# Optimization experiments

Measured on AMD Instinct MI355X. Metric: run time of the kernel, lower is better.

## Reference

```python
import jax, jax.numpy as jnp
import numpy as np

INPUT_DIM, DK, DV = 1024, 128, 128


def setup_inputs() -> dict:
    key = jax.random.key(0)
    ks = jax.random.split(key, 7)
    s = 0.02
    return {
        "x": jax.random.normal(ks[0], (4, 4096, INPUT_DIM), dtype=jnp.float32),
        "Wq": jax.random.normal(ks[1], (INPUT_DIM, DK), dtype=jnp.float32) * s,
        "bq": jnp.zeros((DK,), dtype=jnp.float32),
        "Wk": jax.random.normal(ks[2], (INPUT_DIM, DK), dtype=jnp.float32) * s,
        "bk": jnp.zeros((DK,), dtype=jnp.float32),
        "Wv": jax.random.normal(ks[3], (INPUT_DIM, DV), dtype=jnp.float32) * s,
        "bv": jnp.zeros((DV,), dtype=jnp.float32),
    }


def reference(x, Wq, bq, Wk, bk, Wv, bv):
    # single-head self-attention with explicit QK^T softmax V
    scale = DK ** (-0.5)
    q = x @ Wq + bq          # [b, s, dk]
    k = x @ Wk + bk          # [b, s, dk]
    v = x @ Wv + bv          # [b, s, dv]
    scores = jnp.einsum("bqd,bkd->bqk", q, k) * scale  # [b, s, s]
    attn = jax.nn.softmax(scores, axis=-1)
    return jnp.einsum("bqk,bkd->bqd", attn, v)  # [b, s, dv]
```

## Files before the change

### kernel.cpp

```cpp
#include <hip/hip_runtime.h>
#include <hip/hip_bf16.h>
#include <math.h>
#include <stdint.h>


#define SM_SCALE2 0.1275310225216245f

using f32x4  = __attribute__((ext_vector_type(4))) float;
using f32x16 = __attribute__((ext_vector_type(16))) float;
using bf16x8 = __attribute__((ext_vector_type(8))) short;
using s16x4  = __attribute__((ext_vector_type(4))) short;

#define GLD16(gp, lp) __builtin_amdgcn_global_load_lds(                      \
    (const __attribute__((address_space(1))) void*)(gp),                     \
    (__attribute__((address_space(3))) void*)(lp), 16, 0, 0)

__device__ __forceinline__ short f2bf(float f) {
  union { __hip_bfloat16 h; short s; } u;
  u.h = __float2bfloat16(f);
  return u.s;
}

__global__ __launch_bounds__(256) void wprep_k(const float* __restrict__ Wq,
                                               const float* __restrict__ Wk,
                                               const float* __restrict__ Wv,
                                               short* __restrict__ Wt) {
  int tid = blockIdx.x * 256 + threadIdx.x;
  int mat = tid >> 17;
  int r   = tid & 131071;
  int k   = r >> 7;
  int col = r & 127;
  const float* W = (mat == 0) ? Wq : ((mat == 1) ? Wk : Wv);
  Wt[mat * 131072 + col * 1024 + k] = f2bf(W[k * 128 + col]);
}

__global__ __launch_bounds__(256) void proj_k(const float* __restrict__ x,
                                              const short* __restrict__ Wt,
                                              const float* __restrict__ bq,
                                              const float* __restrict__ bk,
                                              const float* __restrict__ bv,
                                              short* __restrict__ Qb,
                                              short* __restrict__ Kb,
                                              short* __restrict__ Vt) {
  const int r0  = blockIdx.x * 32;
  const int tid  = threadIdx.x;
  const int lane = tid & 63;
  const int w    = tid >> 6;
  const int g    = lane >> 4;
  const int l15  = lane & 15;

  __shared__ __align__(16) char smem[57344];
  const char* Wtb = (const char*)Wt;

  f32x4 acc[3][2][2];
  #pragma unroll
  for (int m = 0; m < 3; ++m)
    #pragma unroll
    for (int rb = 0; rb < 2; ++rb)
      #pragma unroll
      for (int cb = 0; cb < 2; ++cb) acc[m][rb][cb] = (f32x4){0.f, 0.f, 0.f, 0.f};

  const int xrow = tid >> 3;
  const int xsl  = tid & 7;

#define XS(B) (smem + (B) * 4096)
#define WTB   (smem + 8192)

#define STAGE_W(T) do {                                                       \
    _Pragma("unroll")                                                         \
    for (int m = 0; m < 3; ++m)                                               \
      _Pragma("unroll")                                                       \
      for (int c = 0; c < 4; ++c) {                                           \
        const int o  = w * 4096 + c * 1024 + lane * 16;                       \
        const int cr = o >> 7;                                                \
        const int cb = (o >> 4) & 7;                                          \
        GLD16(Wtb + m * 262144 + (size_t)cr * 2048 + (T) * 128 +              \
                  ((cb ^ (cr & 7)) << 4),                                     \
              WTB + m * 16384 + w * 4096 + c * 1024);                         \
      }                                                                       \
  } while (0)

#define LOADX(FX, T) do {                                                     \
    _Pragma("unroll")                                                         \
    for (int p = 0; p < 2; ++p) {                                             \
      const int s = xsl + 8 * p;                                              \
      FX[p] = *(const float4*)(x + (size_t)(r0 + xrow) * 1024 + (T) * 64 + s * 4); \
    }                                                                         \
  } while (0)

#define WRITEX(B, FX) do {                                                    \
    char* xb_ = XS(B);                                                        \
    _Pragma("unroll")                                                         \
    for (int p = 0; p < 2; ++p) {                                             \
      const int s = xsl + 8 * p;                                              \
      s16x4 h = { f2bf(FX[p].x), f2bf(FX[p].y), f2bf(FX[p].z), f2bf(FX[p].w) }; \
      *(s16x4*)(xb_ + xrow * 128 + (((s >> 1) ^ (xrow & 7)) << 4) +           \
                ((s & 1) << 3)) = h;                                          \
    }                                                                         \
  } while (0)

  {
    float4 fx0[2];
    LOADX(fx0, 0);
    WRITEX(0, fx0);
  }
  __syncthreads();
  STAGE_W(0);
  __syncthreads();

  for (int t = 0; t < 16; ++t) {
    const int cur = t & 1;
    float4 fx[2];
    if (t < 15) LOADX(fx, t + 1);

    const char* xb = XS(cur);
    #pragma unroll
    for (int kc = 0; kc < 2; ++kc) {
      bf16x8 a[2];
      #pragma unroll
      for (int rb = 0; rb < 2; ++rb)
        a[rb] = *(const bf16x8*)(xb + (rb * 16 + l15) * 128 +
                                 ((((kc << 2) + g) ^ (l15 & 7)) << 4));
      #pragma unroll
      for (int m = 0; m < 3; ++m)
        #pragma unroll
        for (int cb = 0; cb < 2; ++cb) {
          const int col = w * 32 + cb * 16 + l15;
          bf16x8 b = *(const bf16x8*)(WTB + m * 16384 + col * 128 +
                                      ((((kc << 2) + g) ^ (col & 7)) << 4));
          #pragma unroll
          for (int rb = 0; rb < 2; ++rb)
            acc[m][rb][cb] = __builtin_amdgcn_mfma_f32_16x16x32_bf16(a[rb], b,
                                                                     acc[m][rb][cb], 0, 0, 0);
        }
    }

    if (t < 15) {
      WRITEX(cur ^ 1, fx);
      __syncthreads();
      STAGE_W(t + 1);
      __syncthreads();
    }
  }
#undef STAGE_W
#undef LOADX
#undef WRITEX
#undef XS
#undef WTB

  #pragma unroll
  for (int m = 0; m < 2; ++m) {
    short* dst = (m == 0) ? Qb : Kb;
    const float* bias = (m == 0) ? bq : bk;
    #pragma unroll
    for (int cb = 0; cb < 2; ++cb) {
      const int col = w * 32 + cb * 16 + l15;
      const float bc = bias[col];
      #pragma unroll
      for (int rb = 0; rb < 2; ++rb)
        #pragma unroll
        for (int r = 0; r < 4; ++r) {
          float v = acc[m][rb][cb][r] + bc;
          if (m == 0) v *= SM_SCALE2;
          dst[(size_t)(r0 + rb * 16 + (g << 2) + r) * 128 + col] = f2bf(v);
        }
    }
  }
  __syncthreads();
  {
    short* tb = (short*)smem;
    #pragma unroll
    for (int cb = 0; cb < 2; ++cb) {
      const int col = w * 32 + cb * 16 + l15;
      const float bc = bv[col];
      #pragma unroll
      for (int rb = 0; rb < 2; ++rb)
        #pragma unroll
        for (int r = 0; r < 4; ++r)
          tb[col * 40 + rb * 16 + (g << 2) + r] = f2bf(acc[2][rb][cb][r] + bc);
    }
    __syncthreads();
    const int bb = r0 >> 12;
    const int s0 = r0 & 4095;
    const int d  = tid >> 1;
    #pragma unroll
    for (int j = 0; j < 2; ++j) {
      uint4 vd = *(const uint4*)((char*)tb + d * 80 + (tid & 1) * 32 + j * 16);
      *(uint4*)((char*)Vt +
                ((size_t)(bb * 128 + d) * 4096 + s0 + (tid & 1) * 16 + j * 8) * 2) = vd;
    }
  }
}

__global__ __launch_bounds__(256, 2) void attn_part_k(
    const short* __restrict__ Qb, const short* __restrict__ Kb,
    const short* __restrict__ Vt, float* __restrict__ part,
    float2* __restrict__ ml, float* __restrict__ out, int ns, int direct) {
  const int nwg  = gridDim.x;
  const int bid  = blockIdx.x;
  const int orig = (bid & 7) * (nwg >> 3) + (bid >> 3);
  const int split = orig >> 7;
  const int qb    = orig & 127;
  const int nkt   = 64 / ns;
  const int kt0   = split * nkt;

  const int tid  = threadIdx.x;
  const int lane = tid & 63;
  const int w    = tid >> 6;
  const int l31  = lane & 31;
  const bool hi  = lane >= 32;

  __shared__ __align__(16) char smem[65536];

  const int bb = qb >> 5;
  const size_t qg = (size_t)qb * 128 + w * 32 + l31;

  const char* Kg = (const char*)(Kb + ((size_t)bb << 19));
  const char* Vg = (const char*)(Vt + ((size_t)bb << 19));

  bf16x8 qf[8];
  {
    const short* qp = Qb + qg * 128;
    #pragma unroll
    for (int kd = 0; kd < 8; ++kd)
      qf[kd] = *(const bf16x8*)(qp + 16 * kd + (hi ? 8 : 0));
  }

  float m = -__builtin_inff(), lsum = 0.f;
  f32x16 oacc[4];
  #pragma unroll
  for (int dt = 0; dt < 4; ++dt) oacc[dt] = (f32x16)(0.0f);

#define STAGE(BUF, KT) do {                                                   \
    char* kb_ = smem + (BUF) * 32768;                                         \
    char* vb_ = kb_ + 16384;                                                  \
    _Pragma("unroll")                                                         \
    for (int c = 0; c < 4; ++c) {                                             \
      const int o   = w * 4096 + c * 1024 + lane * 16;                        \
      const int kr  = o >> 8;                                                 \
      const int kc_ = (o >> 4) & 15;                                          \
      GLD16(Kg + (size_t)((KT) * 64 + kr) * 256 + ((kc_ ^ (kr & 15)) << 4),   \
            kb_ + w * 4096 + c * 1024);                                       \
      const int dr  = o >> 7;                                                 \
      const int dc_ = (o >> 4) & 7;                                           \
      GLD16(Vg + (size_t)dr * 8192 + (size_t)(KT) * 128 + ((dc_ ^ (dr & 7)) << 4), \
            vb_ + w * 4096 + c * 1024);                                       \
    }                                                                         \
  } while (0)

  STAGE(0, kt0);
  __syncthreads();

  for (int t = 0; t < nkt; ++t) {
    const int cur = t & 1;
    if (t + 1 < nkt) STAGE(cur ^ 1, kt0 + t + 1);

    const char* KT_ = smem + cur * 32768;
    const char* VT_ = KT_ + 16384;

    f32x16 s0 = (f32x16)(0.0f), s1 = (f32x16)(0.0f);
    __builtin_amdgcn_s_setprio(1);
    #pragma unroll
    for (int kd = 0; kd < 8; ++kd) {
      const int ch = (((2 * kd + (hi ? 1 : 0)) ^ (l31 & 15)) << 4);
      bf16x8 k0 = *(const bf16x8*)(KT_ + l31 * 256 + ch);
      bf16x8 k1 = *(const bf16x8*)(KT_ + (32 + l31) * 256 + ch);
      s0 = __builtin_amdgcn_mfma_f32_32x32x16_bf16(k0, qf[kd], s0, 0, 0, 0);
      s1 = __builtin_amdgcn_mfma_f32_32x32x16_bf16(k1, qf[kd], s1, 0, 0, 0);
    }
    __builtin_amdgcn_s_setprio(0);

    float mx = s0[0];
    #pragma unroll
    for (int i = 1; i < 16; ++i) mx = fmaxf(mx, s0[i]);
    #pragma unroll
    for (int i = 0; i < 16; ++i) mx = fmaxf(mx, s1[i]);
    mx = fmaxf(mx, __shfl_xor(mx, 32));
    if (!__all(mx - m <= 8.f)) {
      const float mn = fmaxf(m, mx);
      const float al = exp2f(m - mn);
      m = mn;
      lsum *= al;
      #pragma unroll
      for (int dt = 0; dt < 4; ++dt)
        #pragma unroll
        for (int i = 0; i < 16; ++i) oacc[dt][i] *= al;
    }
    float rs = 0.f;
    #pragma unroll
    for (int i = 0; i < 16; ++i) { s0[i] = exp2f(s0[i] - m); rs += s0[i]; }
    #pragma unroll
    for (int i = 0; i < 16; ++i) { s1[i] = exp2f(s1[i] - m); rs += s1[i]; }
    rs += __shfl_xor(rs, 32);
    lsum += rs;

    unsigned int W[2][4][2];
    #pragma unroll
    for (int rho = 0; rho < 4; ++rho)
      #pragma unroll
      for (int rh = 0; rh < 2; ++rh) {
        asm("v_cvt_pk_bf16_f32 %0, %1, %2"
            : "=v"(W[0][rho][rh]) : "v"(s0[4 * rho + 2 * rh]), "v"(s0[4 * rho + 2 * rh + 1]));
        asm("v_cvt_pk_bf16_f32 %0, %1, %2"
            : "=v"(W[1][rho][rh]) : "v"(s1[4 * rho + 2 * rh]), "v"(s1[4 * rho + 2 * rh + 1]));
      }

    #pragma unroll
    for (int ks = 0; ks < 4; ++ks) {
      const int t2 = ks >> 1, ksl = ks & 1;
      const unsigned int wl0 = W[t2][2 * ksl][0],     wl1 = W[t2][2 * ksl][1];
      const unsigned int wh0 = W[t2][2 * ksl + 1][0], wh1 = W[t2][2 * ksl + 1][1];
      const unsigned int r0 = __shfl_xor(hi ? wl0 : wh0, 32);
      const unsigned int r1 = __shfl_xor(hi ? wl1 : wh1, 32);
      union { unsigned int u[4]; bf16x8 v; } pb;
      pb.u[0] = hi ? r0 : wl0;
      pb.u[1] = hi ? r1 : wl1;
      pb.u[2] = hi ? wh0 : r0;
      pb.u[3] = hi ? wh1 : r1;
      __builtin_amdgcn_s_setprio(1);
      #pragma unroll
      for (int dt = 0; dt < 4; ++dt) {
        const int row = 32 * dt + l31;
        bf16x8 vf = *(const bf16x8*)(VT_ + row * 128 +
                                     (((2 * ks + (hi ? 1 : 0)) ^ (row & 7)) << 4));
        oacc[dt] = __builtin_amdgcn_mfma_f32_32x32x16_bf16(vf, pb.v, oacc[dt], 0, 0, 0);
      }
      __builtin_amdgcn_s_setprio(0);
    }

    __syncthreads();
  }
#undef STAGE

  const float sc = direct ? (1.f / lsum) : 1.f;
  float* dst = direct ? (out + qg * 128)
                      : (part + ((size_t)split * 16384 + qg) * 128);
  #pragma unroll
  for (int dt = 0; dt < 4; ++dt)
    #pragma unroll
    for (int rq = 0; rq < 4; ++rq) {
      f32x4 v = { oacc[dt][4 * rq + 0] * sc, oacc[dt][4 * rq + 1] * sc,
                  oacc[dt][4 * rq + 2] * sc, oacc[dt][4 * rq + 3] * sc };
      *(f32x4*)(dst + dt * 32 + rq * 8 + (hi ? 4 : 0)) = v;
    }
  if (!direct && lane < 32)
    ml[(size_t)split * 16384 + qg] = make_float2(m, lsum);
}

__global__ __launch_bounds__(256) void merge_k(const float* __restrict__ part,
                                               const float2* __restrict__ ml,
                                               float* __restrict__ out, int ns) {
  const int idx = blockIdx.x * 256 + threadIdx.x;
  const int row = idx >> 5;
  const int c4  = idx & 31;

  float M = -__builtin_inff();
  for (int s = 0; s < ns; ++s) M = fmaxf(M, ml[s * 16384 + row].x);
  float L = 0.f;
  for (int s = 0; s < ns; ++s) {
    const float2 v = ml[s * 16384 + row];
    L += v.y * exp2f(v.x - M);
  }
  const float invL = 1.f / L;

  f32x4 o = (f32x4){0.f, 0.f, 0.f, 0.f};
  for (int s = 0; s < ns; ++s) {
    const float wgt = exp2f(ml[s * 16384 + row].x - M) * invL;
    const f32x4 a = *(const f32x4*)(part + ((size_t)s * 16384 + row) * 128 + c4 * 4);
    o += a * wgt;
  }
  *(f32x4*)(out + (size_t)row * 128 + c4 * 4) = o;
}

extern "C" void kernel_launch(void* const* d_in, const int* in_sizes, int n_in,
                              void* d_out, int out_size, void* d_ws, size_t ws_size,
                              hipStream_t stream) {
  (void)in_sizes; (void)n_in; (void)out_size;
  const float* x  = (const float*)d_in[0];
  const float* Wq = (const float*)d_in[1];
  const float* bq = (const float*)d_in[2];
  const float* Wk = (const float*)d_in[3];
  const float* bk = (const float*)d_in[4];
  const float* Wv = (const float*)d_in[5];
  const float* bv = (const float*)d_in[6];
  float* out = (float*)d_out;

  char* ws = (char*)d_ws;
  short* Wt = (short*)ws;
  short* Qb = (short*)(ws + 786432);
  short* Kb = (short*)(ws + 786432 + 4194304);
  short* Vt = (short*)(ws + 786432 + 2 * 4194304);
  const size_t base = 786432 + 3ull * 4194304;

  const size_t per_split = 16384ull * 128 * 4 + 16384ull * 8;
  int ns = 0;
  if (ws_size >= base + 4 * per_split)      ns = 4;
  else if (ws_size >= base + 2 * per_split) ns = 2;
  const int direct = (ns == 0);
  if (direct) ns = 1;

  float*  part = (float*)(ws + base);
  float2* mlp  = (float2*)(ws + base + (size_t)ns * 16384ull * 128 * 4);

  wprep_k<<<dim3(1536), dim3(256), 0, stream>>>(Wq, Wk, Wv, Wt);
  proj_k<<<dim3(512), dim3(256), 0, stream>>>(x, Wt, bq, bk, bv, Qb, Kb, Vt);
  attn_part_k<<<dim3(128 * ns), dim3(256), 0, stream>>>(Qb, Kb, Vt, part, mlp, out,
                                                        ns, direct);
  if (!direct)
    merge_k<<<dim3(2048), dim3(256), 0, stream>>>(part, mlp, out, ns);
}
```

Measured before the change: 100.9 us.

## Double-buffer weight tiles in projection kernel with smaller K steps

The projection GEMM now double-buffers the weight tiles as well as x, and halves the K step to 32 so that two weight buffers fit in LDS. The async global-to-LDS weight load for the next step is issued before the current MFMAs, and each iteration uses one barrier instead of two. The aim is to hide weight-load latency and cut synchronisation stalls. The cost is twice as many loop iterations with less work per barrier, plus new padded and swizzled LDS layouts that could introduce bank conflicts.

```diff
diff --git a/kernel.cpp b/kernel.cpp
--- a/kernel.cpp
+++ b/kernel.cpp
@@ -49,7 +49,7 @@
   const int g    = lane >> 4;
   const int l15  = lane & 15;
 
-  __shared__ __align__(16) char smem[57344];
+  __shared__ __align__(16) char smem[53760];
   const char* Wtb = (const char*)Wt;
 
   f32x4 acc[3][2][2];
@@ -63,84 +63,72 @@
   const int xrow = tid >> 3;
   const int xsl  = tid & 7;
 
-#define XS(B) (smem + (B) * 4096)
-#define WTB   (smem + 8192)
-
-#define STAGE_W(T) do {                                                       \
+#define XS(B)  (smem + (B) * 2304)
+#define WTB(B) (smem + 4608 + (B) * 24576)
+
+#define STAGE_W(T, B) do {                                                    \
+    char* dstb = WTB(B);                                                      \
     _Pragma("unroll")                                                         \
-    for (int m = 0; m < 3; ++m)                                               \
-      _Pragma("unroll")                                                       \
-      for (int c = 0; c < 4; ++c) {                                           \
-        const int o  = w * 4096 + c * 1024 + lane * 16;                       \
-        const int cr = o >> 7;                                                \
-        const int cb = (o >> 4) & 7;                                          \
-        GLD16(Wtb + m * 262144 + (size_t)cr * 2048 + (T) * 128 +              \
-                  ((cb ^ (cr & 7)) << 4),                                     \
-              WTB + m * 16384 + w * 4096 + c * 1024);                         \
-      }                                                                       \
-  } while (0)
-
-#define LOADX(FX, T) do {                                                     \
-    _Pragma("unroll")                                                         \
-    for (int p = 0; p < 2; ++p) {                                             \
-      const int s = xsl + 8 * p;                                              \
-      FX[p] = *(const float4*)(x + (size_t)(r0 + xrow) * 1024 + (T) * 64 + s * 4); \
+    for (int c = 0; c < 6; ++c) {                                             \
+      const int o    = c * 4096 + tid * 16;                                   \
+      const int m_   = o >> 13;                                               \
+      const int r_   = o & 8191;                                              \
+      const int pr   = r_ >> 7;                                               \
+      const int half = (r_ >> 6) & 1;                                         \
+      const int ch   = (r_ >> 4) & 3;                                         \
+      const int col  = pr * 2 + half;                                         \
+      GLD16(Wtb + m_ * 262144 + (size_t)col * 2048 + (T) * 64 +               \
+                ((ch ^ (pr & 3)) << 4),                                       \
+            dstb + o);                                                        \
     }                                                                         \
   } while (0)
 
+#define LOADX(FX, T)                                                          \
+    FX = *(const float4*)(x + (size_t)(r0 + xrow) * 1024 + (T) * 32 + xsl * 4)
+
 #define WRITEX(B, FX) do {                                                    \
-    char* xb_ = XS(B);                                                        \
-    _Pragma("unroll")                                                         \
-    for (int p = 0; p < 2; ++p) {                                             \
-      const int s = xsl + 8 * p;                                              \
-      s16x4 h = { f2bf(FX[p].x), f2bf(FX[p].y), f2bf(FX[p].z), f2bf(FX[p].w) }; \
-      *(s16x4*)(xb_ + xrow * 128 + (((s >> 1) ^ (xrow & 7)) << 4) +           \
-                ((s & 1) << 3)) = h;                                          \
-    }                                                                         \
+    s16x4 h = { f2bf((FX).x), f2bf((FX).y), f2bf((FX).z), f2bf((FX).w) };     \
+    *(s16x4*)(XS(B) + xrow * 72 + xsl * 8) = h;                               \
   } while (0)
 
   {
-    float4 fx0[2];
+    float4 fx0;
     LOADX(fx0, 0);
     WRITEX(0, fx0);
+    STAGE_W(0, 0);
   }
   __syncthreads();
-  STAGE_W(0);
-  __syncthreads();
-
-  for (int t = 0; t < 16; ++t) {
+
+  for (int t = 0; t < 32; ++t) {
     const int cur = t & 1;
-    float4 fx[2];
-    if (t < 15) LOADX(fx, t + 1);
+    float4 fx;
+    if (t < 31) {
+      LOADX(fx, t + 1);
+      STAGE_W(t + 1, cur ^ 1);
+    }
 
     const char* xb = XS(cur);
-    #pragma unroll
-    for (int kc = 0; kc < 2; ++kc) {
-      bf16x8 a[2];
-      #pragma unroll
-      for (int rb = 0; rb < 2; ++rb)
-        a[rb] = *(const bf16x8*)(xb + (rb * 16 + l15) * 128 +
-                                 ((((kc << 2) + g) ^ (l15 & 7)) << 4));
-      #pragma unroll
-      for (int m = 0; m < 3; ++m)
+    const char* wb = WTB(cur);
+    bf16x8 a[2];
+    #pragma unroll
+    for (int rb = 0; rb < 2; ++rb)
+      a[rb] = *(const bf16x8*)(xb + (rb * 16 + l15) * 72 + g * 16);
+    #pragma unroll
+    for (int m = 0; m < 3; ++m)
+      #pragma unroll
+      for (int cb = 0; cb < 2; ++cb) {
+        const int col = w * 32 + cb * 16 + l15;
+        const int pr  = col >> 1;
+        bf16x8 b = *(const bf16x8*)(wb + m * 8192 + pr * 128 + (col & 1) * 64 +
+                                    ((g ^ (pr & 3)) << 4));
         #pragma unroll
-        for (int cb = 0; cb < 2; ++cb) {
-          const int col = w * 32 + cb * 16 + l15;
-          bf16x8 b = *(const bf16x8*)(WTB + m * 16384 + col * 128 +
-                                      ((((kc << 2) + g) ^ (col & 7)) << 4));
-          #pragma unroll
-          for (int rb = 0; rb < 2; ++rb)
-            acc[m][rb][cb] = __builtin_amdgcn_mfma_f32_16x16x32_bf16(a[rb], b,
-                                                                     acc[m][rb][cb], 0, 0, 0);
-        }
-    }
-
-    if (t < 15) {
-      WRITEX(cur ^ 1, fx);
-      __syncthreads();
-      STAGE_W(t + 1);
-      __syncthreads();
-    }
+        for (int rb = 0; rb < 2; ++rb)
+          acc[m][rb][cb] = __builtin_amdgcn_mfma_f32_16x16x32_bf16(a[rb], b,
+                                                                   acc[m][rb][cb], 0, 0, 0);
+      }
+
+    if (t < 31) WRITEX(cur ^ 1, fx);
+    __syncthreads();
   }
 #undef STAGE_W
 #undef LOADX
```

New measurement: 107.2 us, median of 4. 1.06x slower.

## Load pre-swizzled weight fragments straight into registers instead of staging through LDS

Applied to the files above, without the earlier changes.

The weight-prep kernel now writes W in an MFMA-fragment-ordered layout, so each lane in the projection kernel loads its bf16x8 B operands directly from global memory into registers. This removes the per-iteration LDS staging of W along with one of its two barriers, and shrinks shared memory from 56 KB to 10 KB, which allows more blocks per CU. The main loop is unrolled by two with register double buffering (wfA/wfB) to overlap the global loads with the MFMAs. The cost is 24 extra VGPR-held vectors and weights being re-read from L2 by every wave instead of shared within the block.

```diff
diff --git a/kernel.cpp b/kernel.cpp
--- a/kernel.cpp
+++ b/kernel.cpp
@@ -31,7 +31,10 @@
   int k   = r >> 7;
   int col = r & 127;
   const float* W = (mat == 0) ? Wq : ((mat == 1) ? Wk : Wv);
-  Wt[mat * 131072 + col * 1024 + k] = f2bf(W[k * 128 + col]);
+  const int T = k >> 6, kc = (k >> 5) & 1, g = (k >> 3) & 3, e = k & 7;
+  const int cg = col >> 4, l = col & 15;
+  Wt[((((mat * 16 + T) * 2 + kc) * 8 + cg) << 9) + ((g * 16 + l) << 3) + e] =
+      f2bf(W[k * 128 + col]);
 }
 
 __global__ __launch_bounds__(256) void proj_k(const float* __restrict__ x,
@@ -49,7 +52,7 @@
   const int g    = lane >> 4;
   const int l15  = lane & 15;
 
-  __shared__ __align__(16) char smem[57344];
+  __shared__ __align__(16) char smem[10240];
   const char* Wtb = (const char*)Wt;
 
   f32x4 acc[3][2][2];
@@ -64,20 +67,15 @@
   const int xsl  = tid & 7;
 
 #define XS(B) (smem + (B) * 4096)
-#define WTB   (smem + 8192)
-
-#define STAGE_W(T) do {                                                       \
+
+#define LOADW(DST, T) do {                                                    \
     _Pragma("unroll")                                                         \
-    for (int m = 0; m < 3; ++m)                                               \
-      _Pragma("unroll")                                                       \
-      for (int c = 0; c < 4; ++c) {                                           \
-        const int o  = w * 4096 + c * 1024 + lane * 16;                       \
-        const int cr = o >> 7;                                                \
-        const int cb = (o >> 4) & 7;                                          \
-        GLD16(Wtb + m * 262144 + (size_t)cr * 2048 + (T) * 128 +              \
-                  ((cb ^ (cr & 7)) << 4),                                     \
-              WTB + m * 16384 + w * 4096 + c * 1024);                         \
-      }                                                                       \
+    for (int i = 0; i < 12; ++i) {                                            \
+      const int m_ = i >> 2, cb_ = (i >> 1) & 1, kc_ = i & 1;                 \
+      DST[i] = *(const bf16x8*)(Wtb +                                         \
+          ((((((m_ * 16 + (T)) * 2 + kc_) * 8) + (w * 2 + cb_)) << 10) +      \
+           (lane << 4)));                                                     \
+    }                                                                         \
   } while (0)
 
 #define LOADX(FX, T) do {                                                     \
@@ -99,54 +97,57 @@
     }                                                                         \
   } while (0)
 
+#define COMP(B, WF) do {                                                      \
+    const char* xb = XS(B);                                                   \
+    _Pragma("unroll")                                                         \
+    for (int kc = 0; kc < 2; ++kc) {                                          \
+      bf16x8 a[2];                                                            \
+      _Pragma("unroll")                                                       \
+      for (int rb = 0; rb < 2; ++rb)                                          \
+        a[rb] = *(const bf16x8*)(xb + (rb * 16 + l15) * 128 +                 \
+                                 ((((kc << 2) + g) ^ (l15 & 7)) << 4));       \
+      _Pragma("unroll")                                                       \
+      for (int m = 0; m < 3; ++m)                                             \
+        _Pragma("unroll")                                                     \
+        for (int cb = 0; cb < 2; ++cb)                                        \
+          _Pragma("unroll")                                                   \
+          for (int rb = 0; rb < 2; ++rb)                                      \
+            acc[m][rb][cb] = __builtin_amdgcn_mfma_f32_16x16x32_bf16(         \
+                a[rb], WF[m * 4 + cb * 2 + kc], acc[m][rb][cb], 0, 0, 0);     \
+    }                                                                         \
+  } while (0)
+
+  bf16x8 wfA[12], wfB[12];
+
   {
     float4 fx0[2];
     LOADX(fx0, 0);
     WRITEX(0, fx0);
+    LOADW(wfA, 0);
   }
   __syncthreads();
-  STAGE_W(0);
-  __syncthreads();
-
-  for (int t = 0; t < 16; ++t) {
-    const int cur = t & 1;
+
+  #pragma unroll 1
+  for (int t = 0; t < 16; t += 2) {
     float4 fx[2];
-    if (t < 15) LOADX(fx, t + 1);
-
-    const char* xb = XS(cur);
-    #pragma unroll
-    for (int kc = 0; kc < 2; ++kc) {
-      bf16x8 a[2];
-      #pragma unroll
-      for (int rb = 0; rb < 2; ++rb)
-        a[rb] = *(const bf16x8*)(xb + (rb * 16 + l15) * 128 +
-                                 ((((kc << 2) + g) ^ (l15 & 7)) << 4));
-      #pragma unroll
-      for (int m = 0; m < 3; ++m)
-        #pragma unroll
-        for (int cb = 0; cb < 2; ++cb) {
-          const int col = w * 32 + cb * 16 + l15;
-          bf16x8 b = *(const bf16x8*)(WTB + m * 16384 + col * 128 +
-                                      ((((kc << 2) + g) ^ (col & 7)) << 4));
-          #pragma unroll
-          for (int rb = 0; rb < 2; ++rb)
-            acc[m][rb][cb] = __builtin_amdgcn_mfma_f32_16x16x32_bf16(a[rb], b,
-                                                                     acc[m][rb][cb], 0, 0, 0);
-        }
-    }
-
-    if (t < 15) {
-      WRITEX(cur ^ 1, fx);
-      __syncthreads();
-      STAGE_W(t + 1);
-      __syncthreads();
-    }
-  }
-#undef STAGE_W
+    LOADX(fx, t + 1);
+    LOADW(wfB, t + 1);
+    COMP(0, wfA);
+    WRITEX(1, fx);
+    __syncthreads();
+    if (t + 2 < 16) {
+      LOADX(fx, t + 2);
+      LOADW(wfA, t + 2);
+    }
+    COMP(1, wfB);
+    if (t + 2 < 16) WRITEX(0, fx);
+    __syncthreads();
+  }
+#undef LOADW
 #undef LOADX
 #undef WRITEX
+#undef COMP
 #undef XS
-#undef WTB
 
   #pragma unroll
   for (int m = 0; m < 2; ++m) {
```

Result: faster. 97.60 us (median of 3 runs) (-3.2%).
